# Kernel optimization log

Measured on AMD Instinct MI355X. Metric: run time of the kernel, lower is better.

## Reference

```python
import jax, jax.numpy as jnp
import numpy as np

EPS = 1.1920929e-07  # torch.finfo(float32).eps, F.rms_norm default

def apply_rotary_emb(x, cos, sin):
    # x: [..., L, D]; cos/sin: [L, D//2] broadcast over leading dims
    x1, x2 = jnp.split(x, 2, axis=-1)
    y1 = x1 * cos + x2 * sin
    y2 = -x1 * sin + x2 * cos
    return jnp.concatenate([y1, y2], axis=-1)

def rms_norm(x):
    ms = jnp.mean(jnp.square(x), axis=-1, keepdims=True)
    return x * jax.lax.rsqrt(ms + EPS)

def setup_inputs() -> dict:
    key = jax.random.key(0)
    ks = jax.random.split(key, 7)
    B, L, dim, H = 2, 2048, 2048, 16
    hd = dim // H
    x = jax.random.normal(ks[0], (B, L, dim), dtype=jnp.float32)
    # realistic rotary tables
    inv_freq = 1.0 / (10000.0 ** (np.arange(0, hd, 2, dtype=np.float32) / hd))
    t = np.arange(L, dtype=np.float32)
    ang = jnp.asarray(np.outer(t, inv_freq))  # [L, hd//2]
    cos, sin = jnp.cos(ang), jnp.sin(ang)
    s = 1.0 / np.sqrt(dim)
    wq = jax.random.normal(ks[1], (dim, dim), dtype=jnp.float32) * s
    wk = jax.random.normal(ks[2], (hd, dim), dtype=jnp.float32) * s
    wv = jax.random.normal(ks[3], (hd, dim), dtype=jnp.float32) * s
    wo = jax.random.normal(ks[4], (dim, dim), dtype=jnp.float32) * s
    return {"x": x, "cos": cos, "sin": sin, "wq": wq, "wk": wk, "wv": wv, "wo": wo}

def reference(x, cos, sin, wq, wk, wv, wo):
    B, L, dim = x.shape
    H = 16
    hd = dim // H
    q = jnp.einsum('bld,ed->ble', x, wq).reshape(B, L, H, hd).transpose(0, 2, 1, 3)  # [B,H,L,hd]
    k = jnp.einsum('bld,ed->ble', x, wk)[:, None, :, :]  # [B,1,L,hd]
    v = jnp.einsum('bld,ed->ble', x, wv)[:, None, :, :]
    q = rms_norm(apply_rotary_emb(q, cos, sin))
    k = rms_norm(apply_rotary_emb(k, cos, sin))
    # causal SDPA with MQA broadcast (k,v single head)
    scale = 1.0 / np.sqrt(hd)
    scores = jnp.einsum('bhqd,bokd->bhqk', q, k) * scale  # [B,H,L,L]
    causal = jnp.tril(jnp.ones((L, L), dtype=bool))
    scores = jnp.where(causal, scores, jnp.finfo(scores.dtype).min)
    attn = jax.nn.softmax(scores, axis=-1)
    out = jnp.einsum('bhqk,bokd->bhqd', attn, v)  # [B,H,L,hd]
    out = out.transpose(0, 2, 1, 3).reshape(B, L, dim)
    return jnp.einsum('bld,ed->ble', out, wo)
```

## Files before the change

### kernel.cpp

```cpp
#include <hip/hip_runtime.h>
#include <stdint.h>

typedef short bf16x8 __attribute__((ext_vector_type(8)));
typedef float f32x4  __attribute__((ext_vector_type(4)));
typedef float f32x16 __attribute__((ext_vector_type(16)));
typedef int   i32x2  __attribute__((ext_vector_type(2)));

#define EPS_RMS 1.1920929e-07f
#define INV_SQRT_HD 0.08838834764831845f
#define NEGBIG (-3.0e38f)

__device__ __forceinline__ short f2bf(float f) {
    uint32_t u = __float_as_uint(f);
    u += 0x7fffu + ((u >> 16) & 1u);
    return (short)(u >> 16);
}

__device__ __forceinline__ unsigned int cvtpk(float lo, float hi) {
    unsigned int r;
    asm("v_cvt_pk_bf16_f32 %0, %1, %2" : "=v"(r) : "v"(lo), "v"(hi));
    return r;
}

__device__ __forceinline__ void halfswap(unsigned int a, unsigned int b,
                                         unsigned int& x, unsigned int& y) {
    i32x2 r = __builtin_amdgcn_permlane32_swap((int)a, (int)b, false, false);
    x = (unsigned int)r.x;
    y = (unsigned int)r.y;
}

using gld_t = const __attribute__((address_space(1))) unsigned int*;
using lds_t = __attribute__((address_space(3))) unsigned int*;

__device__ __forceinline__ void glds16(const short* g, short* l) {
    __builtin_amdgcn_global_load_lds((gld_t)g, (lds_t)l, 16, 0, 0);
}

__global__ void cvt_f32_bf16(const float* __restrict__ in, short* __restrict__ out, int n) {
    int i = (blockIdx.x * blockDim.x + threadIdx.x) * 4;
    int stride = gridDim.x * blockDim.x * 4;
    for (; i < n; i += stride) {
        float4 v = *(const float4*)(in + i);
        short4 o;
        o.x = f2bf(v.x); o.y = f2bf(v.y); o.z = f2bf(v.z); o.w = f2bf(v.w);
        *(short4*)(out + i) = o;
    }
}

__global__ __launch_bounds__(512, 4) void gemm_bt(
    const short* __restrict__ A, const short* __restrict__ Bw,
    float* __restrict__ C, int M, int N, int K)
{
    __shared__ short sA[2][128 * 32];
    __shared__ short sB[2][128 * 32];
    const int tid  = threadIdx.x;
    const int lane = tid & 63;
    const int wave = tid >> 6;
    const int wm = (wave >> 1) * 32;
    const int wn = (wave & 1) * 64;
    const size_t row0 = (size_t)blockIdx.y * 128;
    const size_t col0 = (size_t)blockIdx.x * 128;
    const int fr = lane & 15;
    const int fk = (lane >> 4) * 8;

    f32x4 acc[2][4] = {};

    const short* gA = A + (row0 + (tid >> 2)) * (size_t)K + (tid & 3) * 8;
    const short* gB = Bw + (col0 + (tid >> 2)) * (size_t)K + (tid & 3) * 8;
    const int loff = tid * 8;

    glds16(gA, sA[0] + loff);
    glds16(gB, sB[0] + loff);
    __syncthreads();

    int cur = 0;
    for (int k0 = 0; k0 < K; k0 += 32) {
        if (k0 + 32 < K) {
            const int nxt = cur ^ 1;
            glds16(gA + k0 + 32, sA[nxt] + loff);
            glds16(gB + k0 + 32, sB[nxt] + loff);
        }

        bf16x8 af[2], bb[4];
        #pragma unroll
        for (int m = 0; m < 2; ++m)
            af[m] = *(const bf16x8*)(sA[cur] + (wm + m * 16 + fr) * 32 + fk);
        #pragma unroll
        for (int n = 0; n < 4; ++n)
            bb[n] = *(const bf16x8*)(sB[cur] + (wn + n * 16 + fr) * 32 + fk);
        #pragma unroll
        for (int m = 0; m < 2; ++m)
            #pragma unroll
            for (int n = 0; n < 4; ++n)
                acc[m][n] = __builtin_amdgcn_mfma_f32_16x16x32_bf16(af[m], bb[n], acc[m][n], 0, 0, 0);

        __syncthreads();
        cur ^= 1;
    }

    const int cr = (lane >> 4) * 4;
    #pragma unroll
    for (int m = 0; m < 2; ++m)
        #pragma unroll
        for (int n = 0; n < 4; ++n)
            #pragma unroll
            for (int r = 0; r < 4; ++r)
                C[(row0 + wm + m * 16 + cr + r) * N + col0 + wn + n * 16 + fr] = acc[m][n][r];
}

__global__ __launch_bounds__(256, 1) void prep_kernel(
    const float* __restrict__ qkv, const float* __restrict__ cosT,
    const float* __restrict__ sinT, short* __restrict__ qbf,
    short* __restrict__ kpack, short* __restrict__ vpack)
{
    const int row  = blockIdx.x;
    const int b    = row >> 11;
    const int l    = row & 2047;
    const int wave = threadIdx.x >> 6;
    const int lane = threadIdx.x & 63;
    const float* src = qkv + (size_t)row * 2304;
    const float c = cosT[l * 64 + lane];
    const float s = sinT[l * 64 + lane];

    for (int hh = wave; hh < 18; hh += 4) {
        if (hh < 17) {
            const float* base = src + ((hh < 16) ? hh * 128 : 2048);
            float x1 = base[lane];
            float x2 = base[lane + 64];
            float y1 =  x1 * c + x2 * s;
            float y2 = -x1 * s + x2 * c;
            float ss = y1 * y1 + y2 * y2;
            #pragma unroll
            for (int m = 32; m >= 1; m >>= 1) ss += __shfl_xor(ss, m, 64);
            float sc = rsqrtf(ss * (1.0f / 128.0f) + EPS_RMS);
            if (hh < 16) {
                sc *= INV_SQRT_HD;
                short* dst = qbf + ((size_t)(b * 16 + hh) * 2048 + l) * 128;
                dst[lane]      = f2bf(y1 * sc);
                dst[lane + 64] = f2bf(y2 * sc);
            } else {
                const size_t kb = ((size_t)b * 64 + (l >> 5)) * 4096 + (size_t)(l & 31) * 8;
                int d = lane;
                kpack[kb + (d >> 4) * 512 + ((d >> 3) & 1) * 256 + (d & 7)] = f2bf(y1 * sc);
                d = lane + 64;
                kpack[kb + (d >> 4) * 512 + ((d >> 3) & 1) * 256 + (d & 7)] = f2bf(y2 * sc);
            }
        } else {
            const float* base = src + 2176;
            const size_t vb0 = ((size_t)(b * 32 + (l >> 6)) * 16 + ((l >> 4) & 3)) * 512
                             + ((l >> 3) & 1) * 256 + (l & 7);
            int d = lane;
            vpack[vb0 + (size_t)(d >> 5) * 2048 + (size_t)(d & 31) * 8] = f2bf(base[lane]);
            d = lane + 64;
            vpack[vb0 + (size_t)(d >> 5) * 2048 + (size_t)(d & 31) * 8] = f2bf(base[lane + 64]);
        }
    }
}

template<bool MASKED, bool HAVET1>
__device__ __forceinline__ void attn_chunk(
    int j0, int gq, int hi, int lane,
    const short* __restrict__ kpB, const short* __restrict__ vpB,
    const bf16x8 (&qf)[8], f32x16 (&oacc)[4], float& lsum)
{
    union FragU { unsigned int u[4]; bf16x8 v; };

    const short* kt0 = kpB + (size_t)(j0 >> 5) * 4096 + lane * 8;
    const short* vtc = vpB + (size_t)(j0 >> 6) * 8192 + lane * 8;

    bf16x8 k0[8], k1[8];
    #pragma unroll
    for (int s = 0; s < 8; ++s) k0[s] = *(const bf16x8*)(kt0 + s * 512);
    if (HAVET1) {
        #pragma unroll
        for (int s = 0; s < 8; ++s) k1[s] = *(const bf16x8*)(kt0 + 4096 + s * 512);
    }
    bf16x8 v0[8], v1[8];
    #pragma unroll
    for (int dt = 0; dt < 4; ++dt) {
        v0[2 * dt]     = *(const bf16x8*)(vtc + dt * 2048);
        v0[2 * dt + 1] = *(const bf16x8*)(vtc + dt * 2048 + 512);
        if (HAVET1) {
            v1[2 * dt]     = *(const bf16x8*)(vtc + dt * 2048 + 1024);
            v1[2 * dt + 1] = *(const bf16x8*)(vtc + dt * 2048 + 1536);
        }
    }

    f32x16 s0, s1;
    #pragma unroll
    for (int r = 0; r < 16; ++r) s0[r] = 0.f;
    #pragma unroll
    for (int s = 0; s < 8; ++s)
        s0 = __builtin_amdgcn_mfma_f32_32x32x16_bf16(k0[s], qf[s], s0, 0, 0, 0);
    if (HAVET1) {
        #pragma unroll
        for (int r = 0; r < 16; ++r) s1[r] = 0.f;
        #pragma unroll
        for (int s = 0; s < 8; ++s)
            s1 = __builtin_amdgcn_mfma_f32_32x32x16_bf16(k1[s], qf[s], s1, 0, 0, 0);
    }

    if (MASKED) {
        #pragma unroll
        for (int r = 0; r < 16; ++r) {
            const int base = (r & 3) + 8 * (r >> 2) + 4 * hi;
            if (j0 + base > gq) s0[r] = NEGBIG;
            if (HAVET1 && (j0 + 32 + base > gq)) s1[r] = NEGBIG;
        }
    }

    #pragma unroll
    for (int r = 0; r < 16; ++r) {
        s0[r] = __expf(s0[r]);
        if (HAVET1) s1[r] = __expf(s1[r]);
    }

    {
        float a8[8];
        #pragma unroll
        for (int r = 0; r < 8; ++r)
            a8[r] = HAVET1 ? (s0[r] + s0[r + 8]) + (s1[r] + s1[r + 8])
                           : (s0[r] + s0[r + 8]);
        #pragma unroll
        for (int r = 0; r < 4; ++r) a8[r] += a8[r + 4];
        lsum += (a8[0] + a8[1]) + (a8[2] + a8[3]);
    }

    {
        unsigned int W[8];
        #pragma unroll
        for (int jw = 0; jw < 8; ++jw)
            W[jw] = cvtpk(s0[2 * jw], s0[2 * jw + 1]);
        FragU f0, f1;
        halfswap(W[0], W[2], f0.u[0], f0.u[2]);
        halfswap(W[1], W[3], f0.u[1], f0.u[3]);
        halfswap(W[4], W[6], f1.u[0], f1.u[2]);
        halfswap(W[5], W[7], f1.u[1], f1.u[3]);
        #pragma unroll
        for (int dt = 0; dt < 4; ++dt) {
            oacc[dt] = __builtin_amdgcn_mfma_f32_32x32x16_bf16(v0[2 * dt],     f0.v, oacc[dt], 0, 0, 0);
            oacc[dt] = __builtin_amdgcn_mfma_f32_32x32x16_bf16(v0[2 * dt + 1], f1.v, oacc[dt], 0, 0, 0);
        }
    }

    if (HAVET1) {
        unsigned int W[8];
        #pragma unroll
        for (int jw = 0; jw < 8; ++jw)
            W[jw] = cvtpk(s1[2 * jw], s1[2 * jw + 1]);
        FragU f2, f3;
        halfswap(W[0], W[2], f2.u[0], f2.u[2]);
        halfswap(W[1], W[3], f2.u[1], f2.u[3]);
        halfswap(W[4], W[6], f3.u[0], f3.u[2]);
        halfswap(W[5], W[7], f3.u[1], f3.u[3]);
        #pragma unroll
        for (int dt = 0; dt < 4; ++dt) {
            oacc[dt] = __builtin_amdgcn_mfma_f32_32x32x16_bf16(v1[2 * dt],     f2.v, oacc[dt], 0, 0, 0);
            oacc[dt] = __builtin_amdgcn_mfma_f32_32x32x16_bf16(v1[2 * dt + 1], f3.v, oacc[dt], 0, 0, 0);
        }
    }
}

__global__ __launch_bounds__(64, 2) void attn_kernel(
    const short* __restrict__ qbf, const short* __restrict__ kpack,
    const short* __restrict__ vpack, short* __restrict__ obf)
{
    __shared__ short o_sh[32][136];
    const int lane = threadIdx.x & 63;
    const int l31  = lane & 31;
    const int hi   = lane >> 5;

    const int gh = blockIdx.x;
    const int b  = gh >> 4;
    const int h  = gh & 15;
    const int tile = 63 - blockIdx.y;
    const int q0 = tile * 32;
    const int gq = q0 + l31;

    const short* qp  = qbf + ((size_t)gh * 2048 + gq) * 128 + hi * 8;
    const short* kpB = kpack + (size_t)b * 64 * 4096;
    const short* vpB = vpack + (size_t)b * 32 * 8192;

    bf16x8 qf[8];
    #pragma unroll
    for (int s = 0; s < 8; ++s) qf[s] = *(const bf16x8*)(qp + s * 16);

    f32x16 oacc[4];
    #pragma unroll
    for (int dt = 0; dt < 4; ++dt)
        #pragma unroll
        for (int r = 0; r < 16; ++r) oacc[dt][r] = 0.f;
    float lsum = 0.f;

    int j0 = 0;
    for (; j0 < q0 - 32; j0 += 64)
        attn_chunk<false, true>(j0, gq, hi, lane, kpB, vpB, qf, oacc, lsum);
    if (j0 < q0) attn_chunk<true, true >(j0, gq, hi, lane, kpB, vpB, qf, oacc, lsum);
    else         attn_chunk<true, false>(j0, gq, hi, lane, kpB, vpB, qf, oacc, lsum);

    lsum += __shfl_xor(lsum, 32);

    const float inv = 1.0f / lsum;
    #pragma unroll
    for (int dt = 0; dt < 4; ++dt)
        #pragma unroll
        for (int r = 0; r < 16; ++r) {
            const int d = dt * 32 + (r & 3) + 8 * (r >> 2) + 4 * hi;
            o_sh[l31][d] = f2bf(oacc[dt][r] * inv);
        }
    __syncthreads();
    const int rlane = lane >> 4;
    const int dl = (lane & 15) * 8;
    #pragma unroll
    for (int pass = 0; pass < 8; ++pass) {
        const int row = pass * 4 + rlane;
        bf16x8 ov = *(const bf16x8*)(&o_sh[row][dl]);
        *(bf16x8*)(obf + ((size_t)b * 2048 + q0 + row) * 2048 + h * 128 + dl) = ov;
    }
}

extern "C" void kernel_launch(void* const* d_in, const int* in_sizes, int n_in,
                              void* d_out, int out_size, void* d_ws, size_t ws_size,
                              hipStream_t stream)
{
    const float* x    = (const float*)d_in[0];
    const float* cosT = (const float*)d_in[1];
    const float* sinT = (const float*)d_in[2];
    const float* wq   = (const float*)d_in[3];
    const float* wk   = (const float*)d_in[4];
    const float* wv   = (const float*)d_in[5];
    const float* wo   = (const float*)d_in[6];
    float* out = (float*)d_out;

    char* ws = (char*)d_ws;
    size_t off = 0;
    auto alloc = [&](size_t bytes) {
        char* p = ws + off;
        off = (off + bytes + 255) & ~(size_t)255;
        return p;
    };
    short* x_bf  = (short*)alloc((size_t)4096 * 2048 * 2);
    short* wcat  = (short*)alloc((size_t)2304 * 2048 * 2);
    short* wo_bf = (short*)alloc((size_t)2048 * 2048 * 2);
    float* qkv   = (float*)alloc((size_t)4096 * 2304 * 4);
    short* q_bf  = (short*)alloc((size_t)2 * 16 * 2048 * 128 * 2);
    short* kpack = (short*)alloc((size_t)2 * 64 * 4096 * 2);
    short* vpack = (short*)alloc((size_t)2 * 32 * 8192 * 2);
    short* attn_bf = x_bf;
    (void)in_sizes; (void)n_in; (void)out_size; (void)ws_size;

    cvt_f32_bf16<<<1024, 256, 0, stream>>>(x, x_bf, 4096 * 2048);
    cvt_f32_bf16<<<512, 256, 0, stream>>>(wq, wcat, 2048 * 2048);
    cvt_f32_bf16<<<64, 256, 0, stream>>>(wk, wcat + (size_t)2048 * 2048, 128 * 2048);
    cvt_f32_bf16<<<64, 256, 0, stream>>>(wv, wcat + (size_t)2176 * 2048, 128 * 2048);
    cvt_f32_bf16<<<512, 256, 0, stream>>>(wo, wo_bf, 2048 * 2048);

    gemm_bt<<<dim3(18, 32), 512, 0, stream>>>(x_bf, wcat, qkv, 4096, 2304, 2048);

    prep_kernel<<<4096, 256, 0, stream>>>(qkv, cosT, sinT, q_bf, kpack, vpack);

    attn_kernel<<<dim3(32, 64), 64, 0, stream>>>(q_bf, kpack, vpack, attn_bf);

    gemm_bt<<<dim3(16, 32), 512, 0, stream>>>(attn_bf, wo_bf, out, 4096, 2048, 2048);
}
```

Before: 210.9 us.

## Split attention head dimension across two waves per block

The attention kernel now launches 128 threads per block, and each of the two waves accumulates half of the 128-wide output head dimension (two 32-column tiles instead of four). This cuts the number of accumulator registers per wave and doubles the waves available per tile, aiming for higher occupancy and more latency hiding. Both waves redundantly compute the full QK^T scores and softmax sums, so that work is duplicated. The output store is remapped so all 128 threads write rows from shared memory.

Result: slower. 258.5 us (+22.6%).

```diff
diff --git a/kernel.cpp b/kernel.cpp
--- a/kernel.cpp
+++ b/kernel.cpp
@@ -159,9 +159,9 @@
 
 template<bool MASKED, bool HAVET1>
 __device__ __forceinline__ void attn_chunk(
-    int j0, int gq, int hi, int lane,
+    int j0, int gq, int hi, int lane, int dbase,
     const short* __restrict__ kpB, const short* __restrict__ vpB,
-    const bf16x8 (&qf)[8], f32x16 (&oacc)[4], float& lsum)
+    const bf16x8 (&qf)[8], f32x16 (&oacc)[2], float& lsum)
 {
     union FragU { unsigned int u[4]; bf16x8 v; };
 
@@ -175,14 +175,15 @@
         #pragma unroll
         for (int s = 0; s < 8; ++s) k1[s] = *(const bf16x8*)(kt0 + 4096 + s * 512);
     }
-    bf16x8 v0[8], v1[8];
-    #pragma unroll
-    for (int dt = 0; dt < 4; ++dt) {
-        v0[2 * dt]     = *(const bf16x8*)(vtc + dt * 2048);
-        v0[2 * dt + 1] = *(const bf16x8*)(vtc + dt * 2048 + 512);
+    bf16x8 v0[4], v1[4];
+    #pragma unroll
+    for (int t = 0; t < 2; ++t) {
+        const short* vrow = vtc + (size_t)(dbase + t) * 2048;
+        v0[2 * t]     = *(const bf16x8*)(vrow);
+        v0[2 * t + 1] = *(const bf16x8*)(vrow + 512);
         if (HAVET1) {
-            v1[2 * dt]     = *(const bf16x8*)(vtc + dt * 2048 + 1024);
-            v1[2 * dt + 1] = *(const bf16x8*)(vtc + dt * 2048 + 1536);
+            v1[2 * t]     = *(const bf16x8*)(vrow + 1024);
+            v1[2 * t + 1] = *(const bf16x8*)(vrow + 1536);
         }
     }
 
@@ -237,9 +238,9 @@
         halfswap(W[4], W[6], f1.u[0], f1.u[2]);
         halfswap(W[5], W[7], f1.u[1], f1.u[3]);
         #pragma unroll
-        for (int dt = 0; dt < 4; ++dt) {
-            oacc[dt] = __builtin_amdgcn_mfma_f32_32x32x16_bf16(v0[2 * dt],     f0.v, oacc[dt], 0, 0, 0);
-            oacc[dt] = __builtin_amdgcn_mfma_f32_32x32x16_bf16(v0[2 * dt + 1], f1.v, oacc[dt], 0, 0, 0);
+        for (int t = 0; t < 2; ++t) {
+            oacc[t] = __builtin_amdgcn_mfma_f32_32x32x16_bf16(v0[2 * t],     f0.v, oacc[t], 0, 0, 0);
+            oacc[t] = __builtin_amdgcn_mfma_f32_32x32x16_bf16(v0[2 * t + 1], f1.v, oacc[t], 0, 0, 0);
         }
     }
 
@@ -254,21 +255,24 @@
         halfswap(W[4], W[6], f3.u[0], f3.u[2]);
         halfswap(W[5], W[7], f3.u[1], f3.u[3]);
         #pragma unroll
-        for (int dt = 0; dt < 4; ++dt) {
-            oacc[dt] = __builtin_amdgcn_mfma_f32_32x32x16_bf16(v1[2 * dt],     f2.v, oacc[dt], 0, 0, 0);
-            oacc[dt] = __builtin_amdgcn_mfma_f32_32x32x16_bf16(v1[2 * dt + 1], f3.v, oacc[dt], 0, 0, 0);
-        }
-    }
-}
-
-__global__ __launch_bounds__(64, 2) void attn_kernel(
+        for (int t = 0; t < 2; ++t) {
+            oacc[t] = __builtin_amdgcn_mfma_f32_32x32x16_bf16(v1[2 * t],     f2.v, oacc[t], 0, 0, 0);
+            oacc[t] = __builtin_amdgcn_mfma_f32_32x32x16_bf16(v1[2 * t + 1], f3.v, oacc[t], 0, 0, 0);
+        }
+    }
+}
+
+__global__ __launch_bounds__(128, 4) void attn_kernel(
     const short* __restrict__ qbf, const short* __restrict__ kpack,
     const short* __restrict__ vpack, short* __restrict__ obf)
 {
     __shared__ short o_sh[32][136];
-    const int lane = threadIdx.x & 63;
+    const int tid  = threadIdx.x;
+    const int wave = tid >> 6;
+    const int lane = tid & 63;
     const int l31  = lane & 31;
     const int hi   = lane >> 5;
+    const int dbase = wave * 2;
 
     const int gh = blockIdx.x;
     const int b  = gh >> 4;
@@ -285,38 +289,36 @@
     #pragma unroll
     for (int s = 0; s < 8; ++s) qf[s] = *(const bf16x8*)(qp + s * 16);
 
-    f32x16 oacc[4];
-    #pragma unroll
-    for (int dt = 0; dt < 4; ++dt)
-        #pragma unroll
-        for (int r = 0; r < 16; ++r) oacc[dt][r] = 0.f;
+    f32x16 oacc[2];
+    #pragma unroll
+    for (int t = 0; t < 2; ++t)
+        #pragma unroll
+        for (int r = 0; r < 16; ++r) oacc[t][r] = 0.f;
     float lsum = 0.f;
 
     int j0 = 0;
     for (; j0 < q0 - 32; j0 += 64)
-        attn_chunk<false, true>(j0, gq, hi, lane, kpB, vpB, qf, oacc, lsum);
-    if (j0 < q0) attn_chunk<true, true >(j0, gq, hi, lane, kpB, vpB, qf, oacc, lsum);
-    else         attn_chunk<true, false>(j0, gq, hi, lane, kpB, vpB, qf, oacc, lsum);
+        attn_chunk<false, true>(j0, gq, hi, lane, dbase, kpB, vpB, qf, oacc, lsum);
+    if (j0 < q0) attn_chunk<true, true >(j0, gq, hi, lane, dbase, kpB, vpB, qf, oacc, lsum);
+    else         attn_chunk<true, false>(j0, gq, hi, lane, dbase, kpB, vpB, qf, oacc, lsum);
 
     lsum += __shfl_xor(lsum, 32);
 
     const float inv = 1.0f / lsum;
     #pragma unroll
-    for (int dt = 0; dt < 4; ++dt)
+    for (int t = 0; t < 2; ++t)
         #pragma unroll
         for (int r = 0; r < 16; ++r) {
-            const int d = dt * 32 + (r & 3) + 8 * (r >> 2) + 4 * hi;
-            o_sh[l31][d] = f2bf(oacc[dt][r] * inv);
+            const int d = (dbase + t) * 32 + (r & 3) + 8 * (r >> 2) + 4 * hi;
+            o_sh[l31][d] = f2bf(oacc[t][r] * inv);
         }
     __syncthreads();
-    const int rlane = lane >> 4;
-    const int dl = (lane & 15) * 8;
-    #pragma unroll
-    for (int pass = 0; pass < 8; ++pass) {
-        const int row = pass * 4 + rlane;
-        bf16x8 ov = *(const bf16x8*)(&o_sh[row][dl]);
-        *(bf16x8*)(obf + ((size_t)b * 2048 + q0 + row) * 2048 + h * 128 + dl) = ov;
-    }
+    const int orow = tid >> 2;
+    const int od   = (tid & 3) * 32;
+    short* orow_p = obf + ((size_t)b * 2048 + q0 + orow) * 2048 + h * 128 + od;
+    #pragma unroll
+    for (int k = 0; k < 4; ++k)
+        *(bf16x8*)(orow_p + k * 8) = *(const bf16x8*)(&o_sh[orow][od + k * 8]);
 }
 
 extern "C" void kernel_launch(void* const* d_in, const int* in_sizes, int n_in,
@@ -359,7 +361,7 @@
 
     prep_kernel<<<4096, 256, 0, stream>>>(qkv, cosT, sinT, q_bf, kpack, vpack);
 
-    attn_kernel<<<dim3(32, 64), 64, 0, stream>>>(q_bf, kpack, vpack, attn_bf);
+    attn_kernel<<<dim3(32, 64), 128, 0, stream>>>(q_bf, kpack, vpack, attn_bf);
 
     gemm_bt<<<dim3(16, 32), 512, 0, stream>>>(attn_bf, wo_bf, out, 4096, 2048, 2048);
 }
```
